# Performance work log

Hardware: AMD Instinct MI355X
Metric: run time of the kernel (lower is better)

The kernel has to match this reference:

```python
import jax, jax.numpy as jnp
import numpy as np

SR = 16000
N_FFT = 1024
HOP = 160
N_MELS = 160
F_MIN = 50.0
F_MAX = 4000.0
SEG = 32000
N_FREQS = N_FFT // 2 + 1  # 513


def _hz_to_mel(f):
    return 2595.0 * np.log10(1.0 + f / 700.0)


def _mel_to_hz(m):
    return 700.0 * (10.0 ** (m / 2595.0) - 1.0)


def _mel_filterbank():
    # replicates torchaudio melscale_fbanks (htk, norm=None); returns (n_mels, n_freqs)
    all_freqs = np.linspace(0.0, SR / 2.0, N_FREQS)
    m_pts = np.linspace(_hz_to_mel(F_MIN), _hz_to_mel(F_MAX), N_MELS + 2)
    f_pts = _mel_to_hz(m_pts)
    slopes = f_pts[None, :] - all_freqs[:, None]          # (n_freqs, n_mels+2)
    down = -slopes[:, :-2] / (f_pts[1:-1] - f_pts[:-2])
    up = slopes[:, 2:] / (f_pts[2:] - f_pts[1:-1])
    fb = np.maximum(0.0, np.minimum(down, up))            # (n_freqs, n_mels)
    return fb.T.astype(np.float32)


def _dft_matrices():
    k = np.arange(N_FREQS).reshape(-1, 1)
    n = np.arange(N_FFT).reshape(1, -1)
    angle = 2.0 * np.pi * k * n / N_FFT
    return np.cos(angle).astype(np.float32), (-np.sin(angle)).astype(np.float32)


def setup_inputs() -> dict:
    key = jax.random.key(0)
    waveform = jax.random.normal(key, (256, SEG), dtype=jnp.float32)
    # periodic hann window (torch.hann_window default)
    n = np.arange(N_FFT)
    window = (0.5 * (1.0 - np.cos(2.0 * np.pi * n / N_FFT))).astype(np.float32)
    dft_real, dft_imag = _dft_matrices()
    return {
        "waveform": waveform,
        "window": jnp.asarray(window),
        "dft_real": jnp.asarray(dft_real),   # (513, 1024)
        "dft_imag": jnp.asarray(dft_imag),   # (513, 1024)
        "mel_fb": jnp.asarray(_mel_filterbank()),  # (160, 513)
    }


def reference(waveform, window, dft_real, dft_imag, mel_fb):
    pad = N_FFT // 2
    x = jnp.pad(waveform, ((0, 0), (pad, pad)), mode="reflect")  # (B, 33024)
    num_frames = (x.shape[1] - N_FFT) // HOP + 1                  # 201
    idx = np.arange(num_frames)[:, None] * HOP + np.arange(N_FFT)[None, :]
    frames = x[:, idx]                                            # (B, T, n_fft)
    fw = frames * window[None, None, :]
    real = jnp.einsum('btn,fn->btf', fw, dft_real)                # (B, T, 513)
    imag = jnp.einsum('btn,fn->btf', fw, dft_imag)
    power = real * real + imag * imag
    mel = jnp.einsum('btf,mf->btm', power, mel_fb)                # (B, T, n_mels)
    return jnp.transpose(mel, (0, 2, 1))                          # (B, n_mels, T)
```

## Files before the change

### kernel.cpp

```cpp
#include <hip/hip_runtime.h>
#include <stdint.h>

#define NFFT    1024
#define HOP     160
#define NMELS   160
#define SEG     32000
#define PADW    512
#define NFRAMES 201
#define NBATCH  256
#define NSTEP   32
#define ROWB    336
#define NROWS   230
#define WPCH    (NROWS * 21)
#define WPB2    (WPCH * 8)
#define FILLCH  2496

using bf16x8 = __attribute__((ext_vector_type(8))) __bf16;
using f32x4  = __attribute__((ext_vector_type(4))) float;

static __device__ __forceinline__ uint16_t f2bf(float f) {
    union { float f; uint32_t u; } v; v.f = f;
    return (uint16_t)((v.u + 0x7FFFu + ((v.u >> 16) & 1u)) >> 16);
}
static __device__ __forceinline__ void gload16(const void* g, void* l) {
    __builtin_amdgcn_global_load_lds(
        (const __attribute__((address_space(1))) uint32_t*)(uintptr_t)g,
        (__attribute__((address_space(3))) uint32_t*)(uintptr_t)l,
        16, 0, 0);
}

#define PAD_BLKS  (NBATCH * 19)
#define BTF_BLKS  256
#define FBT_BLKS  20
#define PREP_GRID (PAD_BLKS + BTF_BLKS + FBT_BLKS)

__global__ void k_prep(const float* __restrict__ wav, const float* __restrict__ win,
                       const float* __restrict__ dre, const float* __restrict__ dimg,
                       const float* __restrict__ mfb,
                       uint16_t* __restrict__ wp2, uint16_t* __restrict__ BTf,
                       uint16_t* __restrict__ fbT) {
    int bid = blockIdx.x, tid = threadIdx.x;
    if (bid < PAD_BLKS) {
        int b = bid / 19, ib = bid - b * 19;
        int chunk = ib * 256 + tid;
        if (chunk >= WPCH) return;
        int row = chunk / 21, cc = chunk - row * 21;
        uint16_t r[8] = {0,0,0,0,0,0,0,0};
        if (cc < 20) {
            int s0 = row * 160 + cc * 8;
            if (s0 >= PADW && s0 + 8 <= PADW + SEG) {
                const float* s = wav + (size_t)b * SEG + (s0 - PADW);
                float4 v0 = *(const float4*)s;
                float4 v1 = *(const float4*)(s + 4);
                r[0]=f2bf(v0.x); r[1]=f2bf(v0.y); r[2]=f2bf(v0.z); r[3]=f2bf(v0.w);
                r[4]=f2bf(v1.x); r[5]=f2bf(v1.y); r[6]=f2bf(v1.z); r[7]=f2bf(v1.w);
            } else {
                #pragma unroll
                for (int e = 0; e < 8; ++e) {
                    int i = s0 + e - PADW;
                    int j = (i < 0) ? -i : ((i >= SEG) ? (2 * SEG - 2 - i) : i);
                    r[e] = f2bf(wav[(size_t)b * SEG + j]);
                }
            }
        }
        *(uint4*)(wp2 + (size_t)b * WPB2 + (size_t)chunk * 8) = *(const uint4*)r;
    } else if (bid < PAD_BLKS + BTF_BLKS) {
        int idx8 = (bid - PAD_BLKS) * 256 + tid;
        int lane  = idx8 & 63;
        int kstep = (idx8 >> 6) & 31;
        int ntile = (idx8 >> 11) & 15;
        int mat   = idx8 >> 15;
        int bin = ntile * 16 + (lane & 15);
        int k0  = kstep * 32 + (lane >> 4) * 8;
        const float* src = (mat ? dimg : dre) + (size_t)bin * 1024 + k0;
        const float* w   = win + k0;
        uint16_t r[8];
        #pragma unroll
        for (int j = 0; j < 8; ++j) r[j] = f2bf(src[j] * w[j]);
        *(uint4*)(BTf + (size_t)idx8 * 8) = *(const uint4*)r;
    } else {
        int idx = (bid - PAD_BLKS - BTF_BLKS) * 256 + tid;
        if (idx >= 5120) return;
        int lane = idx & 63;
        int fI = idx >> 6;
        int kf = fI & 7, mt = fI >> 3;
        int mel = mt * 16 + (lane & 15);
        int b0  = kf * 32 + (lane >> 4) * 8;
        const float* s = mfb + (size_t)mel * 513 + b0;
        uint16_t r[8];
        #pragma unroll
        for (int j = 0; j < 8; ++j) r[j] = f2bf(s[j]);
        *(uint4*)(fbT + (size_t)idx * 8) = *(const uint4*)r;
    }
}

__global__ __launch_bounds__(1024, 1) void k_main(
    const uint16_t* __restrict__ wp2, const uint16_t* __restrict__ BTf,
    const uint16_t* __restrict__ fbT, float* __restrict__ out)
{
    __shared__ uint4 smem4[57344 / 16];
    char* smem = (char*)smem4;

    const int tid  = threadIdx.x;
    const int lane = tid & 63;
    const int wn   = tid >> 6;
    const int l15 = lane & 15, lg = lane >> 4;
    const int b    = blockIdx.x;
    const int h    = blockIdx.y;
    const int r0   = h ? 96 : 0;

    const uint16_t* wsrc = wp2 + (size_t)b * WPB2 + (size_t)r0 * 168;
    gload16(wsrc + (size_t)tid * 8,          smem + (size_t)tid * 16);
    gload16(wsrc + (size_t)(tid + 1024) * 8, smem + (size_t)(tid + 1024) * 16);
    if (tid < FILLCH - 2048)
        gload16(wsrc + (size_t)(tid + 2048) * 8, smem + (size_t)(tid + 2048) * 16);
    asm volatile("s_waitcnt vmcnt(0)" ::: "memory");
    __syncthreads();

    const uint32_t alane = (uint32_t)(l15 * ROWB + lg * 16);
    const uint16_t* bp = BTf + (size_t)wn * 16384 + lane * 8;

    f32x4 acc[7][2];
    #pragma unroll
    for (int fi = 0; fi < 7; ++fi) {
        acc[fi][0] = f32x4{0.f, 0.f, 0.f, 0.f};
        acc[fi][1] = f32x4{0.f, 0.f, 0.f, 0.f};
    }

    #pragma unroll
    for (int t = 0; t < NSTEP; ++t) {
        bf16x8 bvR = *(const bf16x8*)(bp + (size_t)t * 512);
        bf16x8 bvI = *(const bf16x8*)(bp + 262144 + (size_t)t * 512);
        const uint32_t aoff = (uint32_t)((t / 5) * ROWB + ((32 * t) % 160) * 2);
        bf16x8 av[7];
        #pragma unroll
        for (int fi = 0; fi < 7; ++fi)
            av[fi] = *(const bf16x8*)(smem + alane + aoff + (uint32_t)(fi * 16 * ROWB));
        #pragma unroll
        for (int fi = 0; fi < 7; ++fi) {
            acc[fi][0] = __builtin_amdgcn_mfma_f32_16x16x32_bf16(av[fi], bvR, acc[fi][0], 0, 0, 0);
            acc[fi][1] = __builtin_amdgcn_mfma_f32_16x16x32_bf16(av[fi], bvI, acc[fi][1], 0, 0, 0);
        }
    }
    __syncthreads();

    #pragma unroll
    for (int fi = 0; fi < 7; ++fi)
        #pragma unroll
        for (int e = 0; e < 4; ++e) {
            const int frow = fi * 16 + lg * 4 + e;
            const int bin  = wn * 16 + l15;
            float r = acc[fi][0][e], im = acc[fi][1][e];
            const int slot = ((bin >> 3) + frow) & 31;
            *(uint16_t*)(smem + frow * 512 + slot * 16 + (bin & 7) * 2)
                = f2bf(r * r + im * im);
        }
    __syncthreads();

    float* obase = out + (size_t)b * (NMELS * NFRAMES);
    for (int task = wn; task < 70; task += 16) {
        const int mt = task / 7, ft = task - mt * 7;
        f32x4 d = f32x4{0.f, 0.f, 0.f, 0.f};
        const int frame = ft * 16 + l15;
        #pragma unroll
        for (int kf = 0; kf < 8; ++kf) {
            bf16x8 a = *(const bf16x8*)(fbT + (size_t)((mt * 8 + kf) * 64 + lane) * 8);
            const int slot = (kf * 4 + lg + frame) & 31;
            bf16x8 bb = *(const bf16x8*)(smem + frame * 512 + slot * 16);
            d = __builtin_amdgcn_mfma_f32_16x16x32_bf16(a, bb, d, 0, 0, 0);
        }
        const int fg = r0 + frame;
        const bool own = h ? (fg >= 104 && fg <= 200) : (fg <= 103);
        if (own) {
            #pragma unroll
            for (int e = 0; e < 4; ++e)
                obase[(mt * 16 + lg * 4 + e) * NFRAMES + fg] = d[e];
        }
    }
}

extern "C" void kernel_launch(void* const* d_in, const int* in_sizes, int n_in,
                              void* d_out, int out_size, void* d_ws, size_t ws_size,
                              hipStream_t stream) {
    const float* wav  = (const float*)d_in[0];
    const float* win  = (const float*)d_in[1];
    const float* dre  = (const float*)d_in[2];
    const float* dimg = (const float*)d_in[3];
    const float* mfb  = (const float*)d_in[4];
    float* out = (float*)d_out;

    uint8_t* ws = (uint8_t*)d_ws;
    uint16_t* BTf = (uint16_t*)ws;
    uint16_t* wp2 = (uint16_t*)(ws + (1u << 20));
    size_t off = (1u << 20) + (size_t)NBATCH * WPB2 * 2;
    uint16_t* fbT = (uint16_t*)(ws + off);

    hipLaunchKernelGGL(k_prep, dim3(PREP_GRID), dim3(256), 0, stream,
                       wav, win, dre, dimg, mfb, wp2, BTf, fbT);
    hipLaunchKernelGGL(k_main, dim3(NBATCH, 2), dim3(1024), 0, stream,
                       wp2, BTf, fbT, out);
}
```

Baseline: 80.87 us.

## Split frequency bins across two workgroups and exploit mel filterbank sparsity

The main kernel now runs as 512-thread blocks in a third grid dimension, each covering half of the 256 frequency bins, which raises occupancy and halves per-block LDS. Each half applies only the mel filter rows with nonzero weights in its bin range: mels 0-111 over bins 0-127, and mels 96-159 over bins 128-255. Mel row 111, which straddles the split, is combined with atomicAdd after the prep kernel zeroes it. This relies on the filterbank's sparsity structure, loads the waveform tile twice, and introduces atomics plus an extra output-zeroing pass.

```diff
diff --git a/kernel.cpp b/kernel.cpp
--- a/kernel.cpp
+++ b/kernel.cpp
@@ -31,14 +31,17 @@
 
 #define PAD_BLKS  (NBATCH * 19)
 #define BTF_BLKS  256
-#define FBT_BLKS  20
-#define PREP_GRID (PAD_BLKS + BTF_BLKS + FBT_BLKS)
+#define FBTA_BLKS 7
+#define FBTB_BLKS 4
+#define ZR_BLKS   256
+#define PREP_GRID (PAD_BLKS + BTF_BLKS + FBTA_BLKS + FBTB_BLKS + ZR_BLKS)
 
 __global__ void k_prep(const float* __restrict__ wav, const float* __restrict__ win,
                        const float* __restrict__ dre, const float* __restrict__ dimg,
                        const float* __restrict__ mfb,
                        uint16_t* __restrict__ wp2, uint16_t* __restrict__ BTf,
-                       uint16_t* __restrict__ fbT) {
+                       uint16_t* __restrict__ fbTA, uint16_t* __restrict__ fbTB,
+                       float* __restrict__ out) {
     int bid = blockIdx.x, tid = threadIdx.x;
     if (bid < PAD_BLKS) {
         int b = bid / 19, ib = bid - b * 19;
@@ -78,27 +81,45 @@
         #pragma unroll
         for (int j = 0; j < 8; ++j) r[j] = f2bf(src[j] * w[j]);
         *(uint4*)(BTf + (size_t)idx8 * 8) = *(const uint4*)r;
-    } else {
+    } else if (bid < PAD_BLKS + BTF_BLKS + FBTA_BLKS) {
         int idx = (bid - PAD_BLKS - BTF_BLKS) * 256 + tid;
-        if (idx >= 5120) return;
+        if (idx >= FBTA_BLKS * 256) return;
         int lane = idx & 63;
         int fI = idx >> 6;
-        int kf = fI & 7, mt = fI >> 3;
+        int kf = fI & 3, mt = fI >> 2;
         int mel = mt * 16 + (lane & 15);
-        int b0  = kf * 32 + (lane >> 4) * 8;
-        const float* s = mfb + (size_t)mel * 513 + b0;
+        int bin = kf * 32 + (lane >> 4) * 8;
+        const float* s = mfb + (size_t)mel * 513 + bin;
         uint16_t r[8];
         #pragma unroll
         for (int j = 0; j < 8; ++j) r[j] = f2bf(s[j]);
-        *(uint4*)(fbT + (size_t)idx * 8) = *(const uint4*)r;
-    }
-}
-
-__global__ __launch_bounds__(1024, 1) void k_main(
+        *(uint4*)(fbTA + (size_t)idx * 8) = *(const uint4*)r;
+    } else if (bid < PAD_BLKS + BTF_BLKS + FBTA_BLKS + FBTB_BLKS) {
+        int idx = (bid - PAD_BLKS - BTF_BLKS - FBTA_BLKS) * 256 + tid;
+        if (idx >= FBTB_BLKS * 256) return;
+        int lane = idx & 63;
+        int fI = idx >> 6;
+        int kf = fI & 3, mt = fI >> 2;
+        int mel = 96 + mt * 16 + (lane & 15);
+        int bin = 128 + kf * 32 + (lane >> 4) * 8;
+        const float* s = mfb + (size_t)mel * 513 + bin;
+        uint16_t r[8];
+        #pragma unroll
+        for (int j = 0; j < 8; ++j) r[j] = (mel >= 111) ? f2bf(s[j]) : (uint16_t)0;
+        *(uint4*)(fbTB + (size_t)idx * 8) = *(const uint4*)r;
+    } else {
+        int b = bid - (PAD_BLKS + BTF_BLKS + FBTA_BLKS + FBTB_BLKS);
+        if (tid < NFRAMES)
+            out[(size_t)b * (NMELS * NFRAMES) + 111 * NFRAMES + tid] = 0.f;
+    }
+}
+
+__global__ __launch_bounds__(512, 4) void k_main(
     const uint16_t* __restrict__ wp2, const uint16_t* __restrict__ BTf,
-    const uint16_t* __restrict__ fbT, float* __restrict__ out)
+    const uint16_t* __restrict__ fbTA, const uint16_t* __restrict__ fbTB,
+    float* __restrict__ out)
 {
-    __shared__ uint4 smem4[57344 / 16];
+    __shared__ uint4 smem4[FILLCH];
     char* smem = (char*)smem4;
 
     const int tid  = threadIdx.x;
@@ -107,18 +128,20 @@
     const int l15 = lane & 15, lg = lane >> 4;
     const int b    = blockIdx.x;
     const int h    = blockIdx.y;
+    const int grp  = blockIdx.z;
     const int r0   = h ? 96 : 0;
 
     const uint16_t* wsrc = wp2 + (size_t)b * WPB2 + (size_t)r0 * 168;
-    gload16(wsrc + (size_t)tid * 8,          smem + (size_t)tid * 16);
-    gload16(wsrc + (size_t)(tid + 1024) * 8, smem + (size_t)(tid + 1024) * 16);
+    #pragma unroll
+    for (int i = 0; i < 4; ++i)
+        gload16(wsrc + (size_t)(tid + i * 512) * 8, smem + (size_t)(tid + i * 512) * 16);
     if (tid < FILLCH - 2048)
         gload16(wsrc + (size_t)(tid + 2048) * 8, smem + (size_t)(tid + 2048) * 16);
     asm volatile("s_waitcnt vmcnt(0)" ::: "memory");
     __syncthreads();
 
     const uint32_t alane = (uint32_t)(l15 * ROWB + lg * 16);
-    const uint16_t* bp = BTf + (size_t)wn * 16384 + lane * 8;
+    const uint16_t* bp = BTf + (size_t)(grp * 8 + wn) * 16384 + lane * 8;
 
     f32x4 acc[7][2];
     #pragma unroll
@@ -149,32 +172,39 @@
         #pragma unroll
         for (int e = 0; e < 4; ++e) {
             const int frow = fi * 16 + lg * 4 + e;
-            const int bin  = wn * 16 + l15;
+            const int binl = wn * 16 + l15;
             float r = acc[fi][0][e], im = acc[fi][1][e];
-            const int slot = ((bin >> 3) + frow) & 31;
-            *(uint16_t*)(smem + frow * 512 + slot * 16 + (bin & 7) * 2)
+            const int slot = ((binl >> 3) + frow) & 15;
+            *(uint16_t*)(smem + frow * 256 + slot * 16 + (binl & 7) * 2)
                 = f2bf(r * r + im * im);
         }
     __syncthreads();
 
+    const uint16_t* fbt = grp ? fbTB : fbTA;
+    const int ntask = grp ? 28 : 49;
+    const int mbase = grp ? 96 : 0;
     float* obase = out + (size_t)b * (NMELS * NFRAMES);
-    for (int task = wn; task < 70; task += 16) {
+    for (int task = wn; task < ntask; task += 8) {
         const int mt = task / 7, ft = task - mt * 7;
         f32x4 d = f32x4{0.f, 0.f, 0.f, 0.f};
         const int frame = ft * 16 + l15;
         #pragma unroll
-        for (int kf = 0; kf < 8; ++kf) {
-            bf16x8 a = *(const bf16x8*)(fbT + (size_t)((mt * 8 + kf) * 64 + lane) * 8);
-            const int slot = (kf * 4 + lg + frame) & 31;
-            bf16x8 bb = *(const bf16x8*)(smem + frame * 512 + slot * 16);
+        for (int kf = 0; kf < 4; ++kf) {
+            bf16x8 a = *(const bf16x8*)(fbt + (size_t)((mt * 4 + kf) * 64 + lane) * 8);
+            const int slot = (kf * 4 + lg + frame) & 15;
+            bf16x8 bb = *(const bf16x8*)(smem + frame * 256 + slot * 16);
             d = __builtin_amdgcn_mfma_f32_16x16x32_bf16(a, bb, d, 0, 0, 0);
         }
         const int fg = r0 + frame;
         const bool own = h ? (fg >= 104 && fg <= 200) : (fg <= 103);
         if (own) {
             #pragma unroll
-            for (int e = 0; e < 4; ++e)
-                obase[(mt * 16 + lg * 4 + e) * NFRAMES + fg] = d[e];
+            for (int e = 0; e < 4; ++e) {
+                const int mel = mbase + mt * 16 + lg * 4 + e;
+                float* dst = obase + (size_t)mel * NFRAMES + fg;
+                if (mel == 111)      atomicAdd(dst, d[e]);
+                else if (grp == 0 ? (mel <= 110) : (mel >= 112)) *dst = d[e];
+            }
         }
     }
 }
@@ -193,10 +223,11 @@
     uint16_t* BTf = (uint16_t*)ws;
     uint16_t* wp2 = (uint16_t*)(ws + (1u << 20));
     size_t off = (1u << 20) + (size_t)NBATCH * WPB2 * 2;
-    uint16_t* fbT = (uint16_t*)(ws + off);
+    uint16_t* fbTA = (uint16_t*)(ws + off);
+    uint16_t* fbTB = (uint16_t*)(ws + off + 28672);
 
     hipLaunchKernelGGL(k_prep, dim3(PREP_GRID), dim3(256), 0, stream,
-                       wav, win, dre, dimg, mfb, wp2, BTf, fbT);
-    hipLaunchKernelGGL(k_main, dim3(NBATCH, 2), dim3(1024), 0, stream,
-                       wp2, BTf, fbT, out);
-}
+                       wav, win, dre, dimg, mfb, wp2, BTf, fbTA, fbTB, out);
+    hipLaunchKernelGGL(k_main, dim3(NBATCH, 2, 2), dim3(512), 0, stream,
+                       wp2, BTf, fbTA, fbTB, out);
+}
```

Measured after the change: 75.51 us. 6.6% less time.
